# Kernel tuning notes

Measured on AMD Instinct MI355X. Metric: run time of the kernel, lower is better.

Reference implementation:

```python
import jax, jax.numpy as jnp
import numpy as np

B, T, C = 4, 2048, 1024
H, D = 16, 64  # num_heads, head_dim
P = 64         # prefix length


def setup_inputs() -> dict:
    key = jax.random.key(0)
    ks = jax.random.split(key, 12)
    s = 1.0 / np.sqrt(C)
    return {
        "x": jax.random.normal(ks[0], (B, T, C), dtype=jnp.float32),
        "attn_mask": jax.random.randint(ks[1], (B, 1, 1, T), 0, 2, dtype=jnp.int32),
        "prefix_k": jax.random.normal(ks[2], (B, H, P, D), dtype=jnp.float32),
        "prefix_v": jax.random.normal(ks[3], (B, H, P, D), dtype=jnp.float32),
        "Wq": jax.random.normal(ks[4], (C, C), dtype=jnp.float32) * s,
        "bq": jnp.zeros((C,), dtype=jnp.float32),
        "Wk": jax.random.normal(ks[5], (C, C), dtype=jnp.float32) * s,
        "bk": jnp.zeros((C,), dtype=jnp.float32),
        "Wv": jax.random.normal(ks[6], (C, C), dtype=jnp.float32) * s,
        "bv": jnp.zeros((C,), dtype=jnp.float32),
        "Wo": jax.random.normal(ks[7], (C, C), dtype=jnp.float32) * s,
        "bo": jnp.zeros((C,), dtype=jnp.float32),
    }


def _heads(y):
    # [B,T,C] -> [B,H,T,D]
    return y.reshape(B, T, H, D).transpose(0, 2, 1, 3)


def reference(x, attn_mask, prefix_k, prefix_v, Wq, bq, Wk, bk, Wv, bv, Wo, bo):
    q = _heads(x @ Wq.T + bq)
    k = _heads(x @ Wk.T + bk)
    v = _heads(x @ Wv.T + bv)
    # concat prefix K/V along key dim -> [B,H,P+T,D]
    k = jnp.concatenate([prefix_k, k], axis=2)
    v = jnp.concatenate([prefix_v, v], axis=2)
    # prefix positions are always visible
    prefix_mask = jnp.ones((B, 1, 1, P), dtype=attn_mask.dtype)
    mask = jnp.concatenate([prefix_mask, attn_mask], axis=-1)  # [B,1,1,P+T]
    scores = jnp.einsum('bhtd,bhsd->bhts', q, k) / jnp.sqrt(jnp.asarray(D, x.dtype))
    scores = jnp.where(mask == 0, -jnp.inf, scores)
    w = jax.nn.softmax(scores, axis=-1)
    o = jnp.einsum('bhts,bhsd->bhtd', w, v)
    o = o.transpose(0, 2, 1, 3).reshape(B, T, C)
    return o @ Wo.T + bo
```

## Files before the change

### kernel.cpp

```cpp
#include <hip/hip_runtime.h>
#include <hip/hip_bf16.h>

typedef __bf16 bf16;
typedef __attribute__((ext_vector_type(8))) __bf16 bf16x8;
typedef __attribute__((ext_vector_type(4))) __bf16 bf16x4;
typedef __attribute__((ext_vector_type(4))) float f32x4;
typedef __attribute__((ext_vector_type(16))) float f32x16;

#define MFMA16(a, b, c) __builtin_amdgcn_mfma_f32_16x16x32_bf16(a, b, c, 0, 0, 0)
#define MFMA32(a, b, c) __builtin_amdgcn_mfma_f32_32x32x16_bf16(a, b, c, 0, 0, 0)

__device__ __forceinline__ void gl_lds16(const void* g, void* l) {
    __builtin_amdgcn_global_load_lds(
        (const __attribute__((address_space(1))) void*)g,
        (__attribute__((address_space(3))) void*)l, 16, 0, 0);
}

#define BARRIER() do { asm volatile("" ::: "memory"); \
    __builtin_amdgcn_s_barrier(); asm volatile("" ::: "memory"); } while (0)

#define QSCALE 0.18033688011f
#define LOGBIAS 24.0f

__device__ __forceinline__ int vsig4(int c) {
    return ((c >> 4) << 4) + (((c >> 3) & 1) << 2) + ((c & 4) ? 8 : 0);
}

__global__ __launch_bounds__(256) void prep(
    const float* __restrict__ x, const float* __restrict__ Wq,
    const float* __restrict__ Wk, const float* __restrict__ Wv,
    const float* __restrict__ Wo, const float* __restrict__ pk,
    const float* __restrict__ pv, const int* __restrict__ mask,
    bf16* __restrict__ xb, bf16* __restrict__ wb,
    bf16* __restrict__ k_ws, bf16* __restrict__ vt_ws,
    int* __restrict__ ridx, int* __restrict__ nkv)
{
    const int blk = blockIdx.x, tid = threadIdx.x;
    if (blk < 4) {
        const int b = blk, lane = tid & 63, wv = tid >> 6;
        const int* mb = mask + b * 2048;
        int loc[8], s = 0;
#pragma unroll
        for (int e = 0; e < 8; ++e) { loc[e] = (mb[tid * 8 + e] != 0); s += loc[e]; }
        int inc = s;
#pragma unroll
        for (int off = 1; off < 64; off <<= 1) {
            int t = __shfl_up(inc, off);
            if (lane >= off) inc += t;
        }
        __shared__ int wt[4];
        if (lane == 63) wt[wv] = inc;
        __syncthreads();
        int wo = 0;
        for (int w = 0; w < wv; ++w) wo += wt[w];
        int excl = wo + inc - s;
#pragma unroll
        for (int e = 0; e < 8; ++e) {
            if (loc[e]) ridx[b * 2048 + excl] = tid * 8 + e;
            excl += loc[e];
        }
        if (tid == 255) nkv[b] = 64 + wo + inc;
    } else if (blk < 260) {
        int i = (blk - 4) * 256 + tid;
        {
            int base = i * 4;
            int bh = base >> 12, rem = base & 4095;
            float4 a = *(const float4*)&pk[base];
            bf16x4 ab;
            ab[0] = (bf16)a.x; ab[1] = (bf16)a.y; ab[2] = (bf16)a.z; ab[3] = (bf16)a.w;
            *(bf16x4*)&k_ws[(size_t)bh * (2112 * 64) + rem] = ab;
        }
        {
            int bh = i >> 10, r = i & 1023;
            int d = r >> 4, sq = (r & 15) * 4;
            bf16x4 vb;
#pragma unroll
            for (int e = 0; e < 4; ++e)
                vb[e] = (bf16)pv[(size_t)bh * 4096 + (sq + e) * 64 + d];
            *(bf16x4*)&vt_ws[((size_t)bh * 64 + d) * 2112 + vsig4(sq)] = vb;
        }
    } else {
        int i8 = (blk - 260) * 256 + tid;
        const float* src; bf16* dst; size_t off;
        if (i8 < 1048576) { src = x; dst = xb; off = (size_t)i8; }
        else {
            int j = i8 - 1048576;
            int sel = j >> 17;
            off = (size_t)(j & 131071);
            src = (sel == 0) ? Wq : (sel == 1) ? Wk : (sel == 2) ? Wv : Wo;
            dst = wb + (size_t)sel * 1048576;
        }
        float4 a = *(const float4*)&src[off * 8];
        float4 c = *(const float4*)&src[off * 8 + 4];
        bf16x8 o;
        o[0] = (bf16)a.x; o[1] = (bf16)a.y; o[2] = (bf16)a.z; o[3] = (bf16)a.w;
        o[4] = (bf16)c.x; o[5] = (bf16)c.y; o[6] = (bf16)c.z; o[7] = (bf16)c.w;
        *(bf16x8*)&dst[off * 8] = o;
    }
}

__device__ __forceinline__ void gemm_pipe_256x128(
    const bf16* a0, const bf16* a1, const bf16* a2, const bf16* a3,
    const bf16* b0, const bf16* b1,
    bf16* lds, const int wave, const int lane, f32x4 (&acc)[4][4])
{
    const int ln = lane & 15, quad = lane >> 4;
    const int wm = wave >> 1, wn = wave & 1;
    const int so = wave * 512;
    const int aBase = (wm * 64 + ln) * 64;
    const int bBase = 16384 + (wn * 64 + ln) * 64;
    const int c0 = (quad * 8) ^ ((ln & 7) << 3);
    const int c1 = (32 + quad * 8) ^ ((ln & 7) << 3);

    gl_lds16(a0, lds + so);
    gl_lds16(a1, lds + 4096 + so);
    gl_lds16(a2, lds + 8192 + so);
    gl_lds16(a3, lds + 12288 + so);
    gl_lds16(b0, lds + 16384 + so);
    gl_lds16(b1, lds + 20480 + so);

#pragma unroll 2
    for (int t = 0; t < 16; ++t) {
        bf16* cur = lds + ((t & 1) ? 24576 : 0);
        bf16* nxt = lds + ((t & 1) ? 0 : 24576);
        const int kn = (t + 1) * 64;

        if (t < 15) {
            gl_lds16(a0 + kn, nxt + so);
            gl_lds16(a1 + kn, nxt + 4096 + so);
            gl_lds16(a2 + kn, nxt + 8192 + so);
            asm volatile("s_waitcnt vmcnt(3)" ::: "memory");
        } else {
            asm volatile("s_waitcnt vmcnt(0)" ::: "memory");
        }
        BARRIER();

        bf16x8 fa[4][2], fb[2][2];
#pragma unroll
        for (int mi = 0; mi < 4; ++mi) {
            fa[mi][0] = *(const bf16x8*)(cur + aBase + mi * 1024 + c0);
            fa[mi][1] = *(const bf16x8*)(cur + aBase + mi * 1024 + c1);
        }
#pragma unroll
        for (int ni = 0; ni < 2; ++ni) {
            fb[ni][0] = *(const bf16x8*)(cur + bBase + ni * 1024 + c0);
            fb[ni][1] = *(const bf16x8*)(cur + bBase + ni * 1024 + c1);
        }
        __builtin_amdgcn_s_setprio(1);
#pragma unroll
        for (int mi = 0; mi < 4; ++mi)
#pragma unroll
            for (int ni = 0; ni < 2; ++ni) {
                acc[mi][ni] = MFMA16(fa[mi][0], fb[ni][0], acc[mi][ni]);
                acc[mi][ni] = MFMA16(fa[mi][1], fb[ni][1], acc[mi][ni]);
            }
        __builtin_amdgcn_s_setprio(0);
        BARRIER();

#pragma unroll
        for (int ni = 0; ni < 2; ++ni) {
            fb[ni][0] = *(const bf16x8*)(cur + bBase + (2 + ni) * 1024 + c0);
            fb[ni][1] = *(const bf16x8*)(cur + bBase + (2 + ni) * 1024 + c1);
        }
        if (t < 15) {
            gl_lds16(a3 + kn, nxt + 12288 + so);
            gl_lds16(b0 + kn, nxt + 16384 + so);
            gl_lds16(b1 + kn, nxt + 20480 + so);
        }
        BARRIER();
        __builtin_amdgcn_s_setprio(1);
#pragma unroll
        for (int mi = 0; mi < 4; ++mi)
#pragma unroll
            for (int ni = 0; ni < 2; ++ni) {
                acc[mi][2 + ni] = MFMA16(fa[mi][0], fb[ni][0], acc[mi][2 + ni]);
                acc[mi][2 + ni] = MFMA16(fa[mi][1], fb[ni][1], acc[mi][2 + ni]);
            }
        __builtin_amdgcn_s_setprio(0);
        BARRIER();
    }
}

__global__ __launch_bounds__(512, 2) void proj_gemm(
    const bf16* __restrict__ X, const bf16* __restrict__ Wb,
    const float* __restrict__ bq, const float* __restrict__ bk,
    const float* __restrict__ bv, const int* __restrict__ ridx,
    const int* __restrict__ nkv,
    bf16* __restrict__ q_ws, bf16* __restrict__ k_ws, bf16* __restrict__ vt_ws)
{
    __shared__ bf16 lds[49152];
    const int hw = blockIdx.x;
    const int bx = (hw & 7) * 96 + (hw >> 3);
    const int tid = threadIdx.x, wave = tid >> 6, lane = tid & 63;
    const int sr8 = lane >> 3;
    const int csw = ((lane & 7) ^ sr8) << 3;

    int kind, m0 = 0, n0, bsel = 0, nvis = 0, mbase = 0;
    const bf16* W;
    const float* bias;
    if (bx < 256) {
        kind = 0; m0 = (bx >> 3) * 256; n0 = (bx & 7) * 128;
        W = Wb; bias = bq;
    } else {
        int j = bx - 256;
        kind = 1 + (j >> 8);
        int r = j & 255;
        bsel = r >> 6;
        int rr = r & 63;
        mbase = (rr >> 3) * 256;
        n0 = (rr & 7) * 128;
        nvis = nkv[bsel] - 64;
        if (mbase >= nvis) return;
        W = Wb + (size_t)kind * 1048576;
        bias = (kind == 1) ? bk : bv;
    }

    const bf16 *a0, *a1, *a2, *a3;
    if (kind == 0) {
        a0 = X + (size_t)(m0 + wave * 8 + sr8) * 1024 + csw;
        a1 = a0 + (size_t)64 * 1024;
        a2 = a0 + (size_t)128 * 1024;
        a3 = a0 + (size_t)192 * 1024;
    } else {
        const int* rb = ridx + bsel * 2048;
        const int nv1 = nvis - 1;
        int g = mbase + wave * 8 + sr8;
        int e0 = (g       < nv1) ? g       : nv1;
        int e1 = (g + 64  < nv1) ? g + 64  : nv1;
        int e2 = (g + 128 < nv1) ? g + 128 : nv1;
        int e3 = (g + 192 < nv1) ? g + 192 : nv1;
        const bf16* Xb = X + (size_t)bsel * 2048 * 1024 + csw;
        a0 = Xb + (size_t)rb[e0] * 1024;
        a1 = Xb + (size_t)rb[e1] * 1024;
        a2 = Xb + (size_t)rb[e2] * 1024;
        a3 = Xb + (size_t)rb[e3] * 1024;
    }
    const bf16* b0 = W + (size_t)(n0 + wave * 8 + sr8) * 1024 + csw;
    const bf16* b1 = b0 + (size_t)64 * 1024;

    const f32x4 z4 = {0.f, 0.f, 0.f, 0.f};
    f32x4 acc[4][4];
#pragma unroll
    for (int i = 0; i < 4; ++i)
#pragma unroll
        for (int j = 0; j < 4; ++j) acc[i][j] = z4;

    gemm_pipe_256x128(a0, a1, a2, a3, b0, b1, lds, wave, lane, acc);

    const int ln = lane & 15, quad = lane >> 4;
    const int wm = wave >> 1, wn = wave & 1;
    if (kind == 0) {
#pragma unroll
        for (int ni = 0; ni < 4; ++ni) {
            const int n = n0 + wn * 64 + ni * 16 + ln;
            const float bb = bias[n];
            const int h = n >> 6, d = n & 63;
#pragma unroll
            for (int mi = 0; mi < 4; ++mi) {
                int m = m0 + wm * 64 + mi * 16 + quad * 4;
                int b = m >> 11, tq = m & 2047;
#pragma unroll
                for (int r = 0; r < 4; ++r)
                    q_ws[((size_t)(b * 16 + h) * 2048 + tq + r) * 64 + d] =
                        (bf16)((acc[mi][ni][r] + bb) * QSCALE);
            }
        }
    } else {
#pragma unroll
        for (int ni = 0; ni < 4; ++ni) {
            const int n = n0 + wn * 64 + ni * 16 + ln;
            const float bb = bias[n];
            const int h = n >> 6, d = n & 63;
            const size_t bh64 = (size_t)(bsel * 16 + h);
#pragma unroll
            for (int mi = 0; mi < 4; ++mi) {
                int ml = mbase + wm * 64 + mi * 16 + quad * 4;
                if (kind == 1) {
#pragma unroll
                    for (int r = 0; r < 4; ++r)
                        if (ml + r < nvis)
                            k_ws[(bh64 * 2112 + 64 + ml + r) * 64 + d] =
                                (bf16)(acc[mi][ni][r] + bb);
                } else {
                    int g0 = 64 + ml;
                    int c0 = g0 & 63;
                    int gcol = (g0 & ~63) + vsig4(c0);
                    if (ml + 3 < nvis) {
                        bf16x4 pb;
#pragma unroll
                        for (int r = 0; r < 4; ++r) pb[r] = (bf16)(acc[mi][ni][r] + bb);
                        *(bf16x4*)&vt_ws[(bh64 * 64 + d) * 2112 + gcol] = pb;
                    } else {
#pragma unroll
                        for (int r = 0; r < 4; ++r)
                            if (ml + r < nvis)
                                vt_ws[(bh64 * 64 + d) * 2112 + gcol + r] =
                                    (bf16)(acc[mi][ni][r] + bb);
                    }
                }
            }
        }
    }
}

__global__ __launch_bounds__(256, 2) void attn_kernel(
    const bf16* __restrict__ Q, const bf16* __restrict__ K,
    const bf16* __restrict__ VT, const int* __restrict__ nk,
    bf16* __restrict__ O)
{
    __shared__ bf16 smem[128 * 72];
    bf16* Ks = smem;
    bf16* Vt = smem + 64 * 72;
    const int tid = threadIdx.x, wave = tid >> 6, lane = tid & 63;
    const int ln = lane & 31, hh = lane >> 5;
    const int hw = blockIdx.x;
    const int bh = (hw & 7) * 8 + ((hw >> 3) & 7);
    const int qx = hw >> 6;
    const int b = bh >> 4, head = bh & 15;
    const bf16* __restrict__ Kb  = K  + (size_t)bh * (2112 * 64);
    const bf16* __restrict__ Vtb = VT + (size_t)bh * (64 * 2112);
    const int nkeys = nk[b];
    const int send = ((nkeys + 63) >> 6) << 6;
    const int qg = qx * 256 + wave * 64 + ln;

    bf16x8 qf0[4], qf1[4];
#pragma unroll
    for (int kt = 0; kt < 4; ++kt) {
        qf0[kt] = *(const bf16x8*)&Q[((size_t)bh * 2048 + qg) * 64 + kt * 16 + hh * 8];
        qf1[kt] = *(const bf16x8*)&Q[((size_t)bh * 2048 + qg + 32) * 64 + kt * 16 + hh * 8];
    }

    f32x16 m24;
#pragma unroll
    for (int r = 0; r < 16; ++r) m24[r] = -LOGBIAS;

    float l0 = 0.f, l1 = 0.f;
    f32x16 acc00, acc01, acc10, acc11;
#pragma unroll
    for (int r = 0; r < 16; ++r) {
        acc00[r] = 0.f; acc01[r] = 0.f; acc10[r] = 0.f; acc11[r] = 0.f;
    }

    const int ks_s = tid >> 3, ks_c = (tid & 7) * 8;
    const int vd = tid >> 3, vs = (tid & 7) * 8;

    bf16x8 kr0, kr1, vr0, vr1;
    kr0 = *(const bf16x8*)&Kb[(size_t)ks_s * 64 + ks_c];
    kr1 = *(const bf16x8*)&Kb[(size_t)(ks_s + 32) * 64 + ks_c];
    vr0 = *(const bf16x8*)&Vtb[(size_t)vd * 2112 + vs];
    vr1 = *(const bf16x8*)&Vtb[(size_t)(vd + 32) * 2112 + vs];

    for (int s0 = 0; s0 < send; s0 += 64) {
        __syncthreads();
        *(bf16x8*)&Ks[ks_s * 72 + ks_c]        = kr0;
        *(bf16x8*)&Ks[(ks_s + 32) * 72 + ks_c] = kr1;
        *(bf16x8*)&Vt[vd * 72 + vs]            = vr0;
        *(bf16x8*)&Vt[(vd + 32) * 72 + vs]     = vr1;
        __syncthreads();

        if (s0 + 64 < send) {
            const int sn = s0 + 64;
            kr0 = *(const bf16x8*)&Kb[(size_t)(sn + ks_s) * 64 + ks_c];
            kr1 = *(const bf16x8*)&Kb[(size_t)(sn + ks_s + 32) * 64 + ks_c];
            vr0 = *(const bf16x8*)&Vtb[(size_t)vd * 2112 + sn + vs];
            vr1 = *(const bf16x8*)&Vtb[(size_t)(vd + 32) * 2112 + sn + vs];
        }

        f32x16 sc0[2], sc1[2];
#pragma unroll
        for (int ts = 0; ts < 2; ++ts) {
            bf16x8 kf = *(const bf16x8*)&Ks[(ts * 32 + ln) * 72 + hh * 8];
            f32x16 sA = MFMA32(kf, qf0[0], m24);
            f32x16 sB = MFMA32(kf, qf1[0], m24);
#pragma unroll
            for (int kt = 1; kt < 4; ++kt) {
                kf = *(const bf16x8*)&Ks[(ts * 32 + ln) * 72 + kt * 16 + hh * 8];
                sA = MFMA32(kf, qf0[kt], sA);
                sB = MFMA32(kf, qf1[kt], sB);
            }
            sc0[ts] = sA; sc1[ts] = sB;
        }

        float rs0 = 0.f, rs1 = 0.f;
        bf16x8 pf0[4], pf1[4];
        if (s0 + 64 <= nkeys) {
#pragma unroll
            for (int ts = 0; ts < 2; ++ts)
#pragma unroll
                for (int rg = 0; rg < 4; ++rg)
#pragma unroll
                    for (int i = 0; i < 4; ++i) {
                        float p0 = __builtin_amdgcn_exp2f(sc0[ts][rg * 4 + i]);
                        float p1 = __builtin_amdgcn_exp2f(sc1[ts][rg * 4 + i]);
                        rs0 += p0; rs1 += p1;
                        pf0[ts * 2 + (rg >> 1)][(rg & 1) * 4 + i] = (bf16)p0;
                        pf1[ts * 2 + (rg >> 1)][(rg & 1) * 4 + i] = (bf16)p1;
                    }
        } else {
#pragma unroll
            for (int ts = 0; ts < 2; ++ts)
#pragma unroll
                for (int rg = 0; rg < 4; ++rg)
#pragma unroll
                    for (int i = 0; i < 4; ++i) {
                        int key = s0 + ts * 32 + rg * 8 + hh * 4 + i;
                        float add = (key < nkeys) ? 0.f : -1e30f;
                        float p0 = __builtin_amdgcn_exp2f(sc0[ts][rg * 4 + i] + add);
                        float p1 = __builtin_amdgcn_exp2f(sc1[ts][rg * 4 + i] + add);
                        rs0 += p0; rs1 += p1;
                        pf0[ts * 2 + (rg >> 1)][(rg & 1) * 4 + i] = (bf16)p0;
                        pf1[ts * 2 + (rg >> 1)][(rg & 1) * 4 + i] = (bf16)p1;
                    }
        }
        l0 += rs0; l1 += rs1;

#pragma unroll
        for (int st = 0; st < 4; ++st) {
            bf16x8 a0 = *(const bf16x8*)&Vt[ln * 72 + st * 16 + hh * 8];
            acc00 = MFMA32(a0, pf0[st], acc00);
            acc10 = MFMA32(a0, pf1[st], acc10);
            bf16x8 a1 = *(const bf16x8*)&Vt[(32 + ln) * 72 + st * 16 + hh * 8];
            acc01 = MFMA32(a1, pf0[st], acc01);
            acc11 = MFMA32(a1, pf1[st], acc11);
        }
    }

    __syncthreads();
    l0 += __shfl_xor(l0, 32);
    l1 += __shfl_xor(l1, 32);
    const float inv0 = 1.0f / l0, inv1 = 1.0f / l1;
    bf16* scratch = smem + wave * (32 * 72);
    const int orow = lane >> 3, oc = (lane & 7) * 8;
    const int qrow0 = qx * 256 + wave * 64;

#pragma unroll
    for (int rg = 0; rg < 4; ++rg) {
        bf16x4 ob;
#pragma unroll
        for (int i = 0; i < 4; ++i) ob[i] = (bf16)(acc00[rg * 4 + i] * inv0);
        *(bf16x4*)&scratch[ln * 72 + rg * 8 + hh * 4] = ob;
#pragma unroll
        for (int i = 0; i < 4; ++i) ob[i] = (bf16)(acc01[rg * 4 + i] * inv0);
        *(bf16x4*)&scratch[ln * 72 + 32 + rg * 8 + hh * 4] = ob;
    }
    __builtin_amdgcn_s_waitcnt(0xC07F);
    __builtin_amdgcn_sched_barrier(0);
#pragma unroll
    for (int pass = 0; pass < 4; ++pass) {
        int ml = pass * 8 + orow;
        bf16x8 ov = *(const bf16x8*)&scratch[ml * 72 + oc];
        *(bf16x8*)&O[((size_t)b * 2048 + qrow0 + ml) * 1024 + head * 64 + oc] = ov;
    }
    __builtin_amdgcn_s_waitcnt(0xC07F);
    __builtin_amdgcn_sched_barrier(0);

#pragma unroll
    for (int rg = 0; rg < 4; ++rg) {
        bf16x4 ob;
#pragma unroll
        for (int i = 0; i < 4; ++i) ob[i] = (bf16)(acc10[rg * 4 + i] * inv1);
        *(bf16x4*)&scratch[ln * 72 + rg * 8 + hh * 4] = ob;
#pragma unroll
        for (int i = 0; i < 4; ++i) ob[i] = (bf16)(acc11[rg * 4 + i] * inv1);
        *(bf16x4*)&scratch[ln * 72 + 32 + rg * 8 + hh * 4] = ob;
    }
    __builtin_amdgcn_s_waitcnt(0xC07F);
    __builtin_amdgcn_sched_barrier(0);
#pragma unroll
    for (int pass = 0; pass < 4; ++pass) {
        int ml = pass * 8 + orow;
        bf16x8 ov = *(const bf16x8*)&scratch[ml * 72 + oc];
        *(bf16x8*)&O[((size_t)b * 2048 + qrow0 + 32 + ml) * 1024 + head * 64 + oc] = ov;
    }
}

__global__ __launch_bounds__(512, 2) void out_proj_gemm(
    const bf16* __restrict__ A, const bf16* __restrict__ W,
    const float* __restrict__ bias, float* __restrict__ out)
{
    __shared__ bf16 lds[49152];
    const int hw = blockIdx.x;
    const int bx = (hw & 7) * 32 + (hw >> 3);
    const int m0 = (bx >> 3) * 256, n0 = (bx & 7) * 128;
    const int tid = threadIdx.x, wave = tid >> 6, lane = tid & 63;
    const int sr8 = lane >> 3;
    const int csw = ((lane & 7) ^ sr8) << 3;

    const bf16* a0 = A + (size_t)(m0 + wave * 8 + sr8) * 1024 + csw;
    const bf16* a1 = a0 + (size_t)64 * 1024;
    const bf16* a2 = a0 + (size_t)128 * 1024;
    const bf16* a3 = a0 + (size_t)192 * 1024;
    const bf16* b0 = W + (size_t)(n0 + wave * 8 + sr8) * 1024 + csw;
    const bf16* b1 = b0 + (size_t)64 * 1024;

    const f32x4 z4 = {0.f, 0.f, 0.f, 0.f};
    f32x4 acc[4][4];
#pragma unroll
    for (int i = 0; i < 4; ++i)
#pragma unroll
        for (int j = 0; j < 4; ++j) acc[i][j] = z4;

    gemm_pipe_256x128(a0, a1, a2, a3, b0, b1, lds, wave, lane, acc);

    const int ln = lane & 15, quad = lane >> 4;
    const int wm = wave >> 1, wn = wave & 1;
#pragma unroll
    for (int ni = 0; ni < 4; ++ni) {
        const int n = n0 + wn * 64 + ni * 16 + ln;
        const float bb = bias[n];
#pragma unroll
        for (int mi = 0; mi < 4; ++mi) {
            int m = m0 + wm * 64 + mi * 16 + quad * 4;
#pragma unroll
            for (int r = 0; r < 4; ++r)
                out[(size_t)(m + r) * 1024 + n] = acc[mi][ni][r] + bb;
        }
    }
}

extern "C" void kernel_launch(void* const* d_in, const int* in_sizes, int n_in,
                              void* d_out, int out_size, void* d_ws, size_t ws_size,
                              hipStream_t stream)
{
    const float* x    = (const float*)d_in[0];
    const int*   mask = (const int*)d_in[1];
    const float* pk   = (const float*)d_in[2];
    const float* pv   = (const float*)d_in[3];
    const float* Wq   = (const float*)d_in[4];
    const float* bq   = (const float*)d_in[5];
    const float* Wk   = (const float*)d_in[6];
    const float* bk   = (const float*)d_in[7];
    const float* Wv   = (const float*)d_in[8];
    const float* bv   = (const float*)d_in[9];
    const float* Wo   = (const float*)d_in[10];
    const float* bo   = (const float*)d_in[11];
    float* out = (float*)d_out;

    bf16* xb    = (bf16*)d_ws;
    bf16* wb    = xb + (size_t)8388608;
    bf16* q_ws  = wb + (size_t)4194304;
    bf16* k_ws  = q_ws + (size_t)8388608;
    bf16* vt_ws = k_ws + (size_t)8650752;
    int*  ridx  = (int*)(vt_ws + (size_t)8650752);
    int*  nkv   = ridx + 4 * 2048;
    bf16* a_ws  = xb;

    prep<<<dim3(6404), 256, 0, stream>>>(x, Wq, Wk, Wv, Wo, pk, pv, mask,
                                         xb, wb, k_ws, vt_ws, ridx, nkv);
    proj_gemm<<<dim3(768), 512, 0, stream>>>(xb, wb, bq, bk, bv, ridx, nkv,
                                             q_ws, k_ws, vt_ws);
    attn_kernel<<<dim3(512), 256, 0, stream>>>(q_ws, k_ws, vt_ws, nkv, a_ws);
    out_proj_gemm<<<dim3(256), 512, 0, stream>>>(a_ws, wb + (size_t)3 * 1048576,
                                                 bo, out);
}
```

Before: 231.7 us.

## Shrink GEMM tiles to 128x128 with 4 waves and restructured prefetch

Replaces the 256x128, 8-wave GEMM pipeline with a 128x128 tile run by 4 waves. Each wave now computes a 4x4 MFMA block per k-step behind a single barrier, with B prefetched into the next buffer and A prefetched two steps ahead into the current buffer. The projection and output GEMMs launch twice as many smaller blocks (1536 and 512), which improves wave fill across CUs but halves the reuse of each loaded tile. Block-to-tile swizzling is also simplified to a plain n-major mapping.

```diff
diff --git a/kernel.cpp b/kernel.cpp
--- a/kernel.cpp
+++ b/kernel.cpp
@@ -99,116 +99,106 @@
     }
 }
 
-__device__ __forceinline__ void gemm_pipe_256x128(
+__device__ __forceinline__ void gemm_tile128(
     const bf16* a0, const bf16* a1, const bf16* a2, const bf16* a3,
-    const bf16* b0, const bf16* b1,
+    const bf16* b0, const bf16* b1, const bf16* b2, const bf16* b3,
     bf16* lds, const int wave, const int lane, f32x4 (&acc)[4][4])
 {
     const int ln = lane & 15, quad = lane >> 4;
     const int wm = wave >> 1, wn = wave & 1;
-    const int so = wave * 512;
-    const int aBase = (wm * 64 + ln) * 64;
-    const int bBase = 16384 + (wn * 64 + ln) * 64;
+    const int soA = wave * 512;
     const int c0 = (quad * 8) ^ ((ln & 7) << 3);
     const int c1 = (32 + quad * 8) ^ ((ln & 7) << 3);
-
-    gl_lds16(a0, lds + so);
-    gl_lds16(a1, lds + 4096 + so);
-    gl_lds16(a2, lds + 8192 + so);
-    gl_lds16(a3, lds + 12288 + so);
-    gl_lds16(b0, lds + 16384 + so);
-    gl_lds16(b1, lds + 20480 + so);
+    const int aBase = (wm * 64 + ln) * 64;
+    const int bBase = 8192 + (wn * 64 + ln) * 64;
+
+    gl_lds16(a0, lds + soA);
+    gl_lds16(a1, lds + 2048 + soA);
+    gl_lds16(a2, lds + 4096 + soA);
+    gl_lds16(a3, lds + 6144 + soA);
+    gl_lds16(b0, lds + 8192 + soA);
+    gl_lds16(b1, lds + 10240 + soA);
+    gl_lds16(b2, lds + 12288 + soA);
+    gl_lds16(b3, lds + 14336 + soA);
+    gl_lds16(a0 + 64, lds + 16384 + soA);
+    gl_lds16(a1 + 64, lds + 16384 + 2048 + soA);
+    gl_lds16(a2 + 64, lds + 16384 + 4096 + soA);
+    gl_lds16(a3 + 64, lds + 16384 + 6144 + soA);
 
 #pragma unroll 2
     for (int t = 0; t < 16; ++t) {
-        bf16* cur = lds + ((t & 1) ? 24576 : 0);
-        bf16* nxt = lds + ((t & 1) ? 0 : 24576);
-        const int kn = (t + 1) * 64;
-
-        if (t < 15) {
-            gl_lds16(a0 + kn, nxt + so);
-            gl_lds16(a1 + kn, nxt + 4096 + so);
-            gl_lds16(a2 + kn, nxt + 8192 + so);
-            asm volatile("s_waitcnt vmcnt(3)" ::: "memory");
-        } else {
-            asm volatile("s_waitcnt vmcnt(0)" ::: "memory");
-        }
+        bf16* cur = lds + ((t & 1) ? 16384 : 0);
+        bf16* nxt = lds + ((t & 1) ? 0 : 16384);
+
+        if (t < 15) asm volatile("s_waitcnt vmcnt(4)" ::: "memory");
+        else        asm volatile("s_waitcnt vmcnt(0)" ::: "memory");
         BARRIER();
 
-        bf16x8 fa[4][2], fb[2][2];
+        bf16x8 fa[4][2], fb[4][2];
 #pragma unroll
         for (int mi = 0; mi < 4; ++mi) {
             fa[mi][0] = *(const bf16x8*)(cur + aBase + mi * 1024 + c0);
             fa[mi][1] = *(const bf16x8*)(cur + aBase + mi * 1024 + c1);
         }
 #pragma unroll
-        for (int ni = 0; ni < 2; ++ni) {
+        for (int ni = 0; ni < 4; ++ni) {
             fb[ni][0] = *(const bf16x8*)(cur + bBase + ni * 1024 + c0);
             fb[ni][1] = *(const bf16x8*)(cur + bBase + ni * 1024 + c1);
         }
+        if (t < 15) {
+            const int kn = (t + 1) * 64;
+            gl_lds16(b0 + kn, nxt + 8192 + soA);
+            gl_lds16(b1 + kn, nxt + 10240 + soA);
+            gl_lds16(b2 + kn, nxt + 12288 + soA);
+            gl_lds16(b3 + kn, nxt + 14336 + soA);
+        }
         __builtin_amdgcn_s_setprio(1);
 #pragma unroll
         for (int mi = 0; mi < 4; ++mi)
 #pragma unroll
-            for (int ni = 0; ni < 2; ++ni) {
+            for (int ni = 0; ni < 4; ++ni) {
                 acc[mi][ni] = MFMA16(fa[mi][0], fb[ni][0], acc[mi][ni]);
                 acc[mi][ni] = MFMA16(fa[mi][1], fb[ni][1], acc[mi][ni]);
             }
         __builtin_amdgcn_s_setprio(0);
         BARRIER();
-
-#pragma unroll
-        for (int ni = 0; ni < 2; ++ni) {
-            fb[ni][0] = *(const bf16x8*)(cur + bBase + (2 + ni) * 1024 + c0);
-            fb[ni][1] = *(const bf16x8*)(cur + bBase + (2 + ni) * 1024 + c1);
-        }
-        if (t < 15) {
-            gl_lds16(a3 + kn, nxt + 12288 + so);
-            gl_lds16(b0 + kn, nxt + 16384 + so);
-            gl_lds16(b1 + kn, nxt + 20480 + so);
-        }
-        BARRIER();
-        __builtin_amdgcn_s_setprio(1);
-#pragma unroll
-        for (int mi = 0; mi < 4; ++mi)
-#pragma unroll
-            for (int ni = 0; ni < 2; ++ni) {
-                acc[mi][2 + ni] = MFMA16(fa[mi][0], fb[ni][0], acc[mi][2 + ni]);
-                acc[mi][2 + ni] = MFMA16(fa[mi][1], fb[ni][1], acc[mi][2 + ni]);
-            }
-        __builtin_amdgcn_s_setprio(0);
-        BARRIER();
-    }
-}
-
-__global__ __launch_bounds__(512, 2) void proj_gemm(
+        if (t < 14) {
+            const int kn = (t + 2) * 64;
+            gl_lds16(a0 + kn, cur + soA);
+            gl_lds16(a1 + kn, cur + 2048 + soA);
+            gl_lds16(a2 + kn, cur + 4096 + soA);
+            gl_lds16(a3 + kn, cur + 6144 + soA);
+        }
+    }
+}
+
+__global__ __launch_bounds__(256, 2) void proj_gemm(
     const bf16* __restrict__ X, const bf16* __restrict__ Wb,
     const float* __restrict__ bq, const float* __restrict__ bk,
     const float* __restrict__ bv, const int* __restrict__ ridx,
     const int* __restrict__ nkv,
     bf16* __restrict__ q_ws, bf16* __restrict__ k_ws, bf16* __restrict__ vt_ws)
 {
-    __shared__ bf16 lds[49152];
+    __shared__ bf16 lds[32768];
     const int hw = blockIdx.x;
-    const int bx = (hw & 7) * 96 + (hw >> 3);
+    const int n0 = (hw & 7) * 128;
+    const int mg = hw >> 3;
     const int tid = threadIdx.x, wave = tid >> 6, lane = tid & 63;
-    const int sr8 = lane >> 3;
-    const int csw = ((lane & 7) ^ sr8) << 3;
-
-    int kind, m0 = 0, n0, bsel = 0, nvis = 0, mbase = 0;
+    const int sr = tid >> 3;
+    const int csw = ((tid & 7) ^ (sr & 7)) << 3;
+
+    int kind, m0 = 0, bsel = 0, nvis = 0, mbase = 0;
     const bf16* W;
     const float* bias;
-    if (bx < 256) {
-        kind = 0; m0 = (bx >> 3) * 256; n0 = (bx & 7) * 128;
+    if (mg < 64) {
+        kind = 0; m0 = mg * 128;
         W = Wb; bias = bq;
     } else {
-        int j = bx - 256;
-        kind = 1 + (j >> 8);
-        int r = j & 255;
-        bsel = r >> 6;
-        int rr = r & 63;
-        mbase = (rr >> 3) * 256;
-        n0 = (rr & 7) * 128;
+        int u = mg - 64;
+        kind = 1 + (u >> 6);
+        int r = u & 63;
+        bsel = r >> 4;
+        mbase = (r & 15) * 128;
         nvis = nkv[bsel] - 64;
         if (mbase >= nvis) return;
         W = Wb + (size_t)kind * 1048576;
@@ -217,26 +207,28 @@
 
     const bf16 *a0, *a1, *a2, *a3;
     if (kind == 0) {
-        a0 = X + (size_t)(m0 + wave * 8 + sr8) * 1024 + csw;
-        a1 = a0 + (size_t)64 * 1024;
-        a2 = a0 + (size_t)128 * 1024;
-        a3 = a0 + (size_t)192 * 1024;
+        a0 = X + (size_t)(m0 + sr) * 1024 + csw;
+        a1 = a0 + (size_t)32 * 1024;
+        a2 = a0 + (size_t)64 * 1024;
+        a3 = a0 + (size_t)96 * 1024;
     } else {
         const int* rb = ridx + bsel * 2048;
         const int nv1 = nvis - 1;
-        int g = mbase + wave * 8 + sr8;
-        int e0 = (g       < nv1) ? g       : nv1;
-        int e1 = (g + 64  < nv1) ? g + 64  : nv1;
-        int e2 = (g + 128 < nv1) ? g + 128 : nv1;
-        int e3 = (g + 192 < nv1) ? g + 192 : nv1;
+        int g = mbase + sr;
+        int e0 = (g      < nv1) ? g      : nv1;
+        int e1 = (g + 32 < nv1) ? g + 32 : nv1;
+        int e2 = (g + 64 < nv1) ? g + 64 : nv1;
+        int e3 = (g + 96 < nv1) ? g + 96 : nv1;
         const bf16* Xb = X + (size_t)bsel * 2048 * 1024 + csw;
         a0 = Xb + (size_t)rb[e0] * 1024;
         a1 = Xb + (size_t)rb[e1] * 1024;
         a2 = Xb + (size_t)rb[e2] * 1024;
         a3 = Xb + (size_t)rb[e3] * 1024;
     }
-    const bf16* b0 = W + (size_t)(n0 + wave * 8 + sr8) * 1024 + csw;
-    const bf16* b1 = b0 + (size_t)64 * 1024;
+    const bf16* b0 = W + (size_t)(n0 + sr) * 1024 + csw;
+    const bf16* b1 = b0 + (size_t)32 * 1024;
+    const bf16* b2 = b0 + (size_t)64 * 1024;
+    const bf16* b3 = b0 + (size_t)96 * 1024;
 
     const f32x4 z4 = {0.f, 0.f, 0.f, 0.f};
     f32x4 acc[4][4];
@@ -245,7 +237,7 @@
 #pragma unroll
         for (int j = 0; j < 4; ++j) acc[i][j] = z4;
 
-    gemm_pipe_256x128(a0, a1, a2, a3, b0, b1, lds, wave, lane, acc);
+    gemm_tile128(a0, a1, a2, a3, b0, b1, b2, b3, lds, wave, lane, acc);
 
     const int ln = lane & 15, quad = lane >> 4;
     const int wm = wave >> 1, wn = wave & 1;
@@ -283,8 +275,8 @@
                                 (bf16)(acc[mi][ni][r] + bb);
                 } else {
                     int g0 = 64 + ml;
-                    int c0 = g0 & 63;
-                    int gcol = (g0 & ~63) + vsig4(c0);
+                    int c0v = g0 & 63;
+                    int gcol = (g0 & ~63) + vsig4(c0v);
                     if (ml + 3 < nvis) {
                         bf16x4 pb;
 #pragma unroll
@@ -474,24 +466,26 @@
     }
 }
 
-__global__ __launch_bounds__(512, 2) void out_proj_gemm(
+__global__ __launch_bounds__(256, 2) void out_proj_gemm(
     const bf16* __restrict__ A, const bf16* __restrict__ W,
     const float* __restrict__ bias, float* __restrict__ out)
 {
-    __shared__ bf16 lds[49152];
+    __shared__ bf16 lds[32768];
     const int hw = blockIdx.x;
-    const int bx = (hw & 7) * 32 + (hw >> 3);
-    const int m0 = (bx >> 3) * 256, n0 = (bx & 7) * 128;
+    const int n0 = (hw & 7) * 128;
+    const int m0 = (hw >> 3) * 128;
     const int tid = threadIdx.x, wave = tid >> 6, lane = tid & 63;
-    const int sr8 = lane >> 3;
-    const int csw = ((lane & 7) ^ sr8) << 3;
-
-    const bf16* a0 = A + (size_t)(m0 + wave * 8 + sr8) * 1024 + csw;
-    const bf16* a1 = a0 + (size_t)64 * 1024;
-    const bf16* a2 = a0 + (size_t)128 * 1024;
-    const bf16* a3 = a0 + (size_t)192 * 1024;
-    const bf16* b0 = W + (size_t)(n0 + wave * 8 + sr8) * 1024 + csw;
-    const bf16* b1 = b0 + (size_t)64 * 1024;
+    const int sr = tid >> 3;
+    const int csw = ((tid & 7) ^ (sr & 7)) << 3;
+
+    const bf16* a0 = A + (size_t)(m0 + sr) * 1024 + csw;
+    const bf16* a1 = a0 + (size_t)32 * 1024;
+    const bf16* a2 = a0 + (size_t)64 * 1024;
+    const bf16* a3 = a0 + (size_t)96 * 1024;
+    const bf16* b0 = W + (size_t)(n0 + sr) * 1024 + csw;
+    const bf16* b1 = b0 + (size_t)32 * 1024;
+    const bf16* b2 = b0 + (size_t)64 * 1024;
+    const bf16* b3 = b0 + (size_t)96 * 1024;
 
     const f32x4 z4 = {0.f, 0.f, 0.f, 0.f};
     f32x4 acc[4][4];
@@ -500,7 +494,7 @@
 #pragma unroll
         for (int j = 0; j < 4; ++j) acc[i][j] = z4;
 
-    gemm_pipe_256x128(a0, a1, a2, a3, b0, b1, lds, wave, lane, acc);
+    gemm_tile128(a0, a1, a2, a3, b0, b1, b2, b3, lds, wave, lane, acc);
 
     const int ln = lane & 15, quad = lane >> 4;
     const int wm = wave >> 1, wn = wave & 1;
@@ -547,9 +541,9 @@
 
     prep<<<dim3(6404), 256, 0, stream>>>(x, Wq, Wk, Wv, Wo, pk, pv, mask,
                                          xb, wb, k_ws, vt_ws, ridx, nkv);
-    proj_gemm<<<dim3(768), 512, 0, stream>>>(xb, wb, bq, bk, bv, ridx, nkv,
-                                             q_ws, k_ws, vt_ws);
+    proj_gemm<<<dim3(1536), 256, 0, stream>>>(xb, wb, bq, bk, bv, ridx, nkv,
+                                              q_ws, k_ws, vt_ws);
     attn_kernel<<<dim3(512), 256, 0, stream>>>(q_ws, k_ws, vt_ws, nkv, a_ws);
-    out_proj_gemm<<<dim3(256), 512, 0, stream>>>(a_ws, wb + (size_t)3 * 1048576,
+    out_proj_gemm<<<dim3(512), 256, 0, stream>>>(a_ws, wb + (size_t)3 * 1048576,
                                                  bo, out);
 }
```

After: 234.8 us. No clear change (+1.3%).

## Switch projection GEMMs to 256x256 tiles with an 8-phase staged LDS pipeline

Applied to the files above, without the earlier changes.

Replaces the 256x128 GEMM main loop with a 256x256 tile in which each wave computes 128x64, doubling per-wave MFMA work per fragment load. Global-to-LDS staging is split into four half-tile groups interleaved with four MFMA phases, with one group prefetched two steps ahead, to overlap memory with compute. The tile change halves the grid sizes of proj_gemm and out_proj_gemm. In exchange it needs 128KB of LDS and doubles the accumulator registers, which may cut occupancy below the declared two blocks per CU. The smaller grid (128 blocks for the output projection) may also underfill the CUs.

```diff
diff --git a/kernel.cpp b/kernel.cpp
--- a/kernel.cpp
+++ b/kernel.cpp
@@ -99,86 +99,122 @@
     }
 }
 
-__device__ __forceinline__ void gemm_pipe_256x128(
-    const bf16* a0, const bf16* a1, const bf16* a2, const bf16* a3,
-    const bf16* b0, const bf16* b1,
-    bf16* lds, const int wave, const int lane, f32x4 (&acc)[4][4])
+__device__ __forceinline__ void gemm_8phase_256(
+    const bf16* aP0, const bf16* aP1, const bf16* aP2, const bf16* aP3,
+    const bf16* bP0, const bf16* bP1, const bf16* bP2, const bf16* bP3,
+    bf16* lds, const int tid, f32x4 (&acc)[8][4])
 {
+    const int wave = tid >> 6, lane = tid & 63;
     const int ln = lane & 15, quad = lane >> 4;
-    const int wm = wave >> 1, wn = wave & 1;
+    const int wm = wave >> 2, wn = wave & 3;
     const int so = wave * 512;
-    const int aBase = (wm * 64 + ln) * 64;
-    const int bBase = 16384 + (wn * 64 + ln) * 64;
-    const int c0 = (quad * 8) ^ ((ln & 7) << 3);
-    const int c1 = (32 + quad * 8) ^ ((ln & 7) << 3);
-
-    gl_lds16(a0, lds + so);
-    gl_lds16(a1, lds + 4096 + so);
-    gl_lds16(a2, lds + 8192 + so);
-    gl_lds16(a3, lds + 12288 + so);
-    gl_lds16(b0, lds + 16384 + so);
-    gl_lds16(b1, lds + 20480 + so);
+    const int aoff = (wm * 128 + ln) * 64;
+    const int boff = 16384 + (wn * 64 + ln) * 64;
+    const int k0c = ((quad    ) ^ (ln & 7)) << 3;
+    const int k1c = ((quad + 4) ^ (ln & 7)) << 3;
+
+#define BUFO(u) (((u) & 1) * 32768)
+#define STG_H0(u) { gl_lds16(aP0 + (u)*64, lds + BUFO(u) + so); \
+                    gl_lds16(aP1 + (u)*64, lds + BUFO(u) + 4096 + so); }
+#define STG_H1(u) { gl_lds16(aP2 + (u)*64, lds + BUFO(u) + 8192 + so); \
+                    gl_lds16(aP3 + (u)*64, lds + BUFO(u) + 12288 + so); }
+#define STG_H2(u) { gl_lds16(bP0 + (u)*64, lds + BUFO(u) + 16384 + so); \
+                    gl_lds16(bP1 + (u)*64, lds + BUFO(u) + 20480 + so); }
+#define STG_H3(u) { gl_lds16(bP2 + (u)*64, lds + BUFO(u) + 24576 + so); \
+                    gl_lds16(bP3 + (u)*64, lds + BUFO(u) + 28672 + so); }
+
+    STG_H0(0); STG_H1(0); STG_H2(0); STG_H3(0);
+    STG_H0(1);
+    asm volatile("s_waitcnt vmcnt(2)" ::: "memory");
+    BARRIER();
 
 #pragma unroll 2
     for (int t = 0; t < 16; ++t) {
-        bf16* cur = lds + ((t & 1) ? 24576 : 0);
-        bf16* nxt = lds + ((t & 1) ? 0 : 24576);
-        const int kn = (t + 1) * 64;
-
-        if (t < 15) {
-            gl_lds16(a0 + kn, nxt + so);
-            gl_lds16(a1 + kn, nxt + 4096 + so);
-            gl_lds16(a2 + kn, nxt + 8192 + so);
-            asm volatile("s_waitcnt vmcnt(3)" ::: "memory");
+        bf16* cur = lds + ((t & 1) ? 32768 : 0);
+        bf16x8 fa[4][2], fb01[2][2], fb23[2][2];
+
+#pragma unroll
+        for (int mi = 0; mi < 4; ++mi) {
+            fa[mi][0] = *(const bf16x8*)(cur + aoff + mi * 1024 + k0c);
+            fa[mi][1] = *(const bf16x8*)(cur + aoff + mi * 1024 + k1c);
+        }
+#pragma unroll
+        for (int ni = 0; ni < 2; ++ni) {
+            fb01[ni][0] = *(const bf16x8*)(cur + boff + ni * 1024 + k0c);
+            fb01[ni][1] = *(const bf16x8*)(cur + boff + ni * 1024 + k1c);
+        }
+        if (t < 15) STG_H1(t + 1);
+        BARRIER();
+        __builtin_amdgcn_s_setprio(1);
+#pragma unroll
+        for (int mi = 0; mi < 4; ++mi)
+#pragma unroll
+            for (int ni = 0; ni < 2; ++ni) {
+                acc[mi][ni] = MFMA16(fa[mi][0], fb01[ni][0], acc[mi][ni]);
+                acc[mi][ni] = MFMA16(fa[mi][1], fb01[ni][1], acc[mi][ni]);
+            }
+        __builtin_amdgcn_s_setprio(0);
+        BARRIER();
+
+#pragma unroll
+        for (int ni = 0; ni < 2; ++ni) {
+            fb23[ni][0] = *(const bf16x8*)(cur + boff + (2 + ni) * 1024 + k0c);
+            fb23[ni][1] = *(const bf16x8*)(cur + boff + (2 + ni) * 1024 + k1c);
+        }
+        if (t < 15) STG_H2(t + 1);
+        BARRIER();
+        __builtin_amdgcn_s_setprio(1);
+#pragma unroll
+        for (int mi = 0; mi < 4; ++mi)
+#pragma unroll
+            for (int ni = 0; ni < 2; ++ni) {
+                acc[mi][2 + ni] = MFMA16(fa[mi][0], fb23[ni][0], acc[mi][2 + ni]);
+                acc[mi][2 + ni] = MFMA16(fa[mi][1], fb23[ni][1], acc[mi][2 + ni]);
+            }
+        __builtin_amdgcn_s_setprio(0);
+        BARRIER();
+
+#pragma unroll
+        for (int mi = 0; mi < 4; ++mi) {
+            fa[mi][0] = *(const bf16x8*)(cur + aoff + (4 + mi) * 1024 + k0c);
+            fa[mi][1] = *(const bf16x8*)(cur + aoff + (4 + mi) * 1024 + k1c);
+        }
+        if (t < 15) STG_H3(t + 1);
+        BARRIER();
+        __builtin_amdgcn_s_setprio(1);
+#pragma unroll
+        for (int mi = 0; mi < 4; ++mi)
+#pragma unroll
+            for (int ni = 0; ni < 2; ++ni) {
+                acc[4 + mi][ni] = MFMA16(fa[mi][0], fb01[ni][0], acc[4 + mi][ni]);
+                acc[4 + mi][ni] = MFMA16(fa[mi][1], fb01[ni][1], acc[4 + mi][ni]);
+            }
+        __builtin_amdgcn_s_setprio(0);
+        BARRIER();
+
+        if (t < 14) {
+            STG_H0(t + 2);
+            asm volatile("s_waitcnt vmcnt(2)" ::: "memory");
         } else {
             asm volatile("s_waitcnt vmcnt(0)" ::: "memory");
         }
         BARRIER();
-
-        bf16x8 fa[4][2], fb[2][2];
-#pragma unroll
-        for (int mi = 0; mi < 4; ++mi) {
-            fa[mi][0] = *(const bf16x8*)(cur + aBase + mi * 1024 + c0);
-            fa[mi][1] = *(const bf16x8*)(cur + aBase + mi * 1024 + c1);
-        }
-#pragma unroll
-        for (int ni = 0; ni < 2; ++ni) {
-            fb[ni][0] = *(const bf16x8*)(cur + bBase + ni * 1024 + c0);
-            fb[ni][1] = *(const bf16x8*)(cur + bBase + ni * 1024 + c1);
-        }
         __builtin_amdgcn_s_setprio(1);
 #pragma unroll
         for (int mi = 0; mi < 4; ++mi)
 #pragma unroll
             for (int ni = 0; ni < 2; ++ni) {
-                acc[mi][ni] = MFMA16(fa[mi][0], fb[ni][0], acc[mi][ni]);
-                acc[mi][ni] = MFMA16(fa[mi][1], fb[ni][1], acc[mi][ni]);
+                acc[4 + mi][2 + ni] = MFMA16(fa[mi][0], fb23[ni][0], acc[4 + mi][2 + ni]);
+                acc[4 + mi][2 + ni] = MFMA16(fa[mi][1], fb23[ni][1], acc[4 + mi][2 + ni]);
             }
         __builtin_amdgcn_s_setprio(0);
         BARRIER();
-
-#pragma unroll
-        for (int ni = 0; ni < 2; ++ni) {
-            fb[ni][0] = *(const bf16x8*)(cur + bBase + (2 + ni) * 1024 + c0);
-            fb[ni][1] = *(const bf16x8*)(cur + bBase + (2 + ni) * 1024 + c1);
-        }
-        if (t < 15) {
-            gl_lds16(a3 + kn, nxt + 12288 + so);
-            gl_lds16(b0 + kn, nxt + 16384 + so);
-            gl_lds16(b1 + kn, nxt + 20480 + so);
-        }
-        BARRIER();
-        __builtin_amdgcn_s_setprio(1);
-#pragma unroll
-        for (int mi = 0; mi < 4; ++mi)
-#pragma unroll
-            for (int ni = 0; ni < 2; ++ni) {
-                acc[mi][2 + ni] = MFMA16(fa[mi][0], fb[ni][0], acc[mi][2 + ni]);
-                acc[mi][2 + ni] = MFMA16(fa[mi][1], fb[ni][1], acc[mi][2 + ni]);
-            }
-        __builtin_amdgcn_s_setprio(0);
-        BARRIER();
-    }
+    }
+#undef BUFO
+#undef STG_H0
+#undef STG_H1
+#undef STG_H2
+#undef STG_H3
 }
 
 __global__ __launch_bounds__(512, 2) void proj_gemm(
@@ -188,27 +224,27 @@
     const int* __restrict__ nkv,
     bf16* __restrict__ q_ws, bf16* __restrict__ k_ws, bf16* __restrict__ vt_ws)
 {
-    __shared__ bf16 lds[49152];
+    __shared__ bf16 lds[65536];
     const int hw = blockIdx.x;
-    const int bx = (hw & 7) * 96 + (hw >> 3);
-    const int tid = threadIdx.x, wave = tid >> 6, lane = tid & 63;
-    const int sr8 = lane >> 3;
-    const int csw = ((lane & 7) ^ sr8) << 3;
-
-    int kind, m0 = 0, n0, bsel = 0, nvis = 0, mbase = 0;
+    const int bx = (hw & 7) * 48 + (hw >> 3);
+    const int tid = threadIdx.x;
+    const int sr = tid >> 3;
+    const int csw = ((tid & 7) ^ (sr & 7)) << 3;
+
+    int kind, m0 = 0, bsel = 0, nvis = 0, mbase = 0, n0;
     const bf16* W;
     const float* bias;
-    if (bx < 256) {
-        kind = 0; m0 = (bx >> 3) * 256; n0 = (bx & 7) * 128;
+    if (bx < 128) {
+        kind = 0; m0 = (bx >> 2) * 256; n0 = (bx & 3) * 256;
         W = Wb; bias = bq;
     } else {
-        int j = bx - 256;
-        kind = 1 + (j >> 8);
-        int r = j & 255;
-        bsel = r >> 6;
-        int rr = r & 63;
-        mbase = (rr >> 3) * 256;
-        n0 = (rr & 7) * 128;
+        int u = bx - 128;
+        kind = 1 + (u >> 7);
+        int r = u & 127;
+        bsel = r >> 5;
+        int rr = r & 31;
+        mbase = (rr >> 2) * 256;
+        n0 = (rr & 3) * 256;
         nvis = nkv[bsel] - 64;
         if (mbase >= nvis) return;
         W = Wb + (size_t)kind * 1048576;
@@ -217,14 +253,14 @@
 
     const bf16 *a0, *a1, *a2, *a3;
     if (kind == 0) {
-        a0 = X + (size_t)(m0 + wave * 8 + sr8) * 1024 + csw;
+        a0 = X + (size_t)(m0 + sr) * 1024 + csw;
         a1 = a0 + (size_t)64 * 1024;
         a2 = a0 + (size_t)128 * 1024;
         a3 = a0 + (size_t)192 * 1024;
     } else {
         const int* rb = ridx + bsel * 2048;
         const int nv1 = nvis - 1;
-        int g = mbase + wave * 8 + sr8;
+        int g = mbase + sr;
         int e0 = (g       < nv1) ? g       : nv1;
         int e1 = (g + 64  < nv1) ? g + 64  : nv1;
         int e2 = (g + 128 < nv1) ? g + 128 : nv1;
@@ -235,20 +271,23 @@
         a2 = Xb + (size_t)rb[e2] * 1024;
         a3 = Xb + (size_t)rb[e3] * 1024;
     }
-    const bf16* b0 = W + (size_t)(n0 + wave * 8 + sr8) * 1024 + csw;
+    const bf16* b0 = W + (size_t)(n0 + sr) * 1024 + csw;
     const bf16* b1 = b0 + (size_t)64 * 1024;
+    const bf16* b2 = b0 + (size_t)128 * 1024;
+    const bf16* b3 = b0 + (size_t)192 * 1024;
 
     const f32x4 z4 = {0.f, 0.f, 0.f, 0.f};
-    f32x4 acc[4][4];
-#pragma unroll
-    for (int i = 0; i < 4; ++i)
+    f32x4 acc[8][4];
+#pragma unroll
+    for (int i = 0; i < 8; ++i)
 #pragma unroll
         for (int j = 0; j < 4; ++j) acc[i][j] = z4;
 
-    gemm_pipe_256x128(a0, a1, a2, a3, b0, b1, lds, wave, lane, acc);
-
+    gemm_8phase_256(a0, a1, a2, a3, b0, b1, b2, b3, lds, tid, acc);
+
+    const int wave = tid >> 6, lane = tid & 63;
     const int ln = lane & 15, quad = lane >> 4;
-    const int wm = wave >> 1, wn = wave & 1;
+    const int wm = wave >> 2, wn = wave & 3;
     if (kind == 0) {
 #pragma unroll
         for (int ni = 0; ni < 4; ++ni) {
@@ -256,8 +295,8 @@
             const float bb = bias[n];
             const int h = n >> 6, d = n & 63;
 #pragma unroll
-            for (int mi = 0; mi < 4; ++mi) {
-                int m = m0 + wm * 64 + mi * 16 + quad * 4;
+            for (int mi = 0; mi < 8; ++mi) {
+                int m = m0 + wm * 128 + mi * 16 + quad * 4;
                 int b = m >> 11, tq = m & 2047;
 #pragma unroll
                 for (int r = 0; r < 4; ++r)
@@ -273,8 +312,8 @@
             const int h = n >> 6, d = n & 63;
             const size_t bh64 = (size_t)(bsel * 16 + h);
 #pragma unroll
-            for (int mi = 0; mi < 4; ++mi) {
-                int ml = mbase + wm * 64 + mi * 16 + quad * 4;
+            for (int mi = 0; mi < 8; ++mi) {
+                int ml = mbase + wm * 128 + mi * 16 + quad * 4;
                 if (kind == 1) {
 #pragma unroll
                     for (int r = 0; r < 4; ++r)
@@ -283,8 +322,8 @@
                                 (bf16)(acc[mi][ni][r] + bb);
                 } else {
                     int g0 = 64 + ml;
-                    int c0 = g0 & 63;
-                    int gcol = (g0 & ~63) + vsig4(c0);
+                    int c0v = g0 & 63;
+                    int gcol = (g0 & ~63) + vsig4(c0v);
                     if (ml + 3 < nvis) {
                         bf16x4 pb;
 #pragma unroll
@@ -478,39 +517,42 @@
     const bf16* __restrict__ A, const bf16* __restrict__ W,
     const float* __restrict__ bias, float* __restrict__ out)
 {
-    __shared__ bf16 lds[49152];
+    __shared__ bf16 lds[65536];
     const int hw = blockIdx.x;
-    const int bx = (hw & 7) * 32 + (hw >> 3);
-    const int m0 = (bx >> 3) * 256, n0 = (bx & 7) * 128;
-    const int tid = threadIdx.x, wave = tid >> 6, lane = tid & 63;
-    const int sr8 = lane >> 3;
-    const int csw = ((lane & 7) ^ sr8) << 3;
-
-    const bf16* a0 = A + (size_t)(m0 + wave * 8 + sr8) * 1024 + csw;
+    const int bx = (hw & 7) * 16 + (hw >> 3);
+    const int m0 = (bx >> 2) * 256, n0 = (bx & 3) * 256;
+    const int tid = threadIdx.x;
+    const int sr = tid >> 3;
+    const int csw = ((tid & 7) ^ (sr & 7)) << 3;
+
+    const bf16* a0 = A + (size_t)(m0 + sr) * 1024 + csw;
     const bf16* a1 = a0 + (size_t)64 * 1024;
     const bf16* a2 = a0 + (size_t)128 * 1024;
     const bf16* a3 = a0 + (size_t)192 * 1024;
-    const bf16* b0 = W + (size_t)(n0 + wave * 8 + sr8) * 1024 + csw;
+    const bf16* b0 = W + (size_t)(n0 + sr) * 1024 + csw;
     const bf16* b1 = b0 + (size_t)64 * 1024;
+    const bf16* b2 = b0 + (size_t)128 * 1024;
+    const bf16* b3 = b0 + (size_t)192 * 1024;
 
     const f32x4 z4 = {0.f, 0.f, 0.f, 0.f};
-    f32x4 acc[4][4];
-#pragma unroll
-    for (int i = 0; i < 4; ++i)
+    f32x4 acc[8][4];
+#pragma unroll
+    for (int i = 0; i < 8; ++i)
 #pragma unroll
         for (int j = 0; j < 4; ++j) acc[i][j] = z4;
 
-    gemm_pipe_256x128(a0, a1, a2, a3, b0, b1, lds, wave, lane, acc);
-
+    gemm_8phase_256(a0, a1, a2, a3, b0, b1, b2, b3, lds, tid, acc);
+
+    const int wave = tid >> 6, lane = tid & 63;
     const int ln = lane & 15, quad = lane >> 4;
-    const int wm = wave >> 1, wn = wave & 1;
+    const int wm = wave >> 2, wn = wave & 3;
 #pragma unroll
     for (int ni = 0; ni < 4; ++ni) {
         const int n = n0 + wn * 64 + ni * 16 + ln;
         const float bb = bias[n];
 #pragma unroll
-        for (int mi = 0; mi < 4; ++mi) {
-            int m = m0 + wm * 64 + mi * 16 + quad * 4;
+        for (int mi = 0; mi < 8; ++mi) {
+            int m = m0 + wm * 128 + mi * 16 + quad * 4;
 #pragma unroll
             for (int r = 0; r < 4; ++r)
                 out[(size_t)(m + r) * 1024 + n] = acc[mi][ni][r] + bb;
@@ -547,9 +589,9 @@
 
     prep<<<dim3(6404), 256, 0, stream>>>(x, Wq, Wk, Wv, Wo, pk, pv, mask,
                                          xb, wb, k_ws, vt_ws, ridx, nkv);
-    proj_gemm<<<dim3(768), 512, 0, stream>>>(xb, wb, bq, bk, bv, ridx, nkv,
+    proj_gemm<<<dim3(384), 512, 0, stream>>>(xb, wb, bq, bk, bv, ridx, nkv,
                                              q_ws, k_ws, vt_ws);
     attn_kernel<<<dim3(512), 256, 0, stream>>>(q_ws, k_ws, vt_ws, nkv, a_ws);
-    out_proj_gemm<<<dim3(256), 512, 0, stream>>>(a_ws, wb + (size_t)3 * 1048576,
+    out_proj_gemm<<<dim3(128), 512, 0, stream>>>(a_ws, wb + (size_t)3 * 1048576,
                                                  bo, out);
 }
```

After: 257.4 us. 1.11x slower.
